# Kernel optimization log

Hardware: AMD Instinct MI355X
Metric: run time of the kernel (lower is better)

Reference implementation:

```python
import jax, jax.numpy as jnp
import numpy as np

ALPHA = 0.2  # LeakyReLU negative slope (module init arg)


def setup_inputs() -> dict:
    key = jax.random.key(0)
    ks = jax.random.split(key, 5)
    b, w, K, E = 8, 256, 256, 512  # batch, window_size, n_features, embed (=2*window)
    x = jax.random.normal(ks[0], (b, w, K), dtype=jnp.float32)
    W = jax.random.normal(ks[1], (E, 2 * w), dtype=jnp.float32) * 0.05
    b_lin = jax.random.normal(ks[2], (E,), dtype=jnp.float32) * 0.05
    a = jax.random.normal(ks[3], (E,), dtype=jnp.float32) * 0.05
    bias = jax.random.normal(ks[4], (K, K), dtype=jnp.float32) * 0.05
    return {"x": x, "W": W, "b_lin": b_lin, "a": a, "bias": bias}


def reference(x, W, b_lin, a, bias):
    # x: (b, window, K) -> v: (b, K, window)
    v = jnp.transpose(x, (0, 2, 1))
    w = v.shape[2]
    # lin(concat(v_i, v_j)) == v_i @ Wl^T + v_j @ Wr^T + b_lin  (split weight)
    Wl, Wr = W[:, :w], W[:, w:]
    left = jnp.einsum('bkw,ew->bke', v, Wl)    # (b, K, E)
    right = jnp.einsum('bkw,ew->bke', v, Wr)   # (b, K, E)
    pre = left[:, :, None, :] + right[:, None, :, :] + b_lin  # (b, K, K, E)
    act = jax.nn.leaky_relu(pre, negative_slope=ALPHA)
    e = jnp.einsum('bije,e->bij', act, a) + bias               # (b, K, K)
    attn = jax.nn.softmax(e, axis=2)  # dropout p=0 in eval -> identity
    h = jax.nn.sigmoid(jnp.einsum('bij,bjw->biw', attn, v))    # (b, K, window)
    return jnp.transpose(h, (0, 2, 1))                          # (b, window, K)
```

## Files before the change

### kernel.cpp

```cpp
#include <hip/hip_runtime.h>
#include <math.h>

typedef float f32x4 __attribute__((ext_vector_type(4)));
typedef __bf16 bf16x8 __attribute__((ext_vector_type(8)));
typedef unsigned short u16x8 __attribute__((ext_vector_type(8)));

__device__ __forceinline__ unsigned short f2bf(float f) {
    union { float f; unsigned int u; } v; v.f = f;
    unsigned int u = v.u;
    return (unsigned short)((u + 0x7fffu + ((u >> 16) & 1u)) >> 16);
}
__device__ __forceinline__ float bf_lo(unsigned int d) {
    union { unsigned int u; float f; } v; v.u = d << 16; return v.f;
}
__device__ __forceinline__ float bf_hi(unsigned int d) {
    union { unsigned int u; float f; } v; v.u = d & 0xffff0000u; return v.f;
}
__device__ __forceinline__ float sigmoidf_(float v) {
    return 1.f / (1.f + __expf(-v));
}

__global__ __launch_bounds__(256) void mfma_gemm_kernel(
    const float* __restrict__ x,
    const float* __restrict__ W,
    const float* __restrict__ b_lin,
    float* __restrict__ Lp,
    unsigned short* __restrict__ R2)
{
    const int b = blockIdx.y;
    const int t = blockIdx.x;
    const bool left = (t < 32);
    int m0, n0;
    if (left) { m0 = (t >> 3) * 64; n0 = (t & 7) * 64; }
    else      { const int tt = t - 32; m0 = (tt >> 2) * 64; n0 = (tt & 3) * 64; }

    __shared__ unsigned short As[64][72];
    __shared__ unsigned short Bs[64][72];

    unsigned short (*Ts)[72] = left ? As : Bs;
    unsigned short (*Ds)[72] = left ? Bs : As;
    const int cbase = left ? m0 : n0;
    const int rbase = left ? n0 : m0;
    const int coff  = left ? 0 : 256;

    const int tid  = threadIdx.x;
    const int wv   = tid >> 6;
    const int lane = tid & 63;
    const int wy = wv >> 1, wx = wv & 1;
    const int lr = lane & 15;
    const int lk = lane >> 4;

    const float* xb = x + b * 65536;

    f32x4 acc[2][2];
    #pragma unroll
    for (int i = 0; i < 2; i++)
        #pragma unroll
        for (int jj = 0; jj < 2; jj++) acc[i][jj] = (f32x4){0.f, 0.f, 0.f, 0.f};

    const int wl = tid >> 4;
    const int kg = tid & 15;
    const int dr = tid >> 2;
    const int dc = (tid & 3) * 16;

    for (int k0 = 0; k0 < 256; k0 += 64) {
        #pragma unroll
        for (int p = 0; p < 4; p++) {
            const int w = wl + 16 * p;
            const float4 v = *(const float4*)(xb + (k0 + w) * 256 + cbase + kg * 4);
            Ts[kg * 4 + 0][w] = f2bf(v.x);
            Ts[kg * 4 + 1][w] = f2bf(v.y);
            Ts[kg * 4 + 2][w] = f2bf(v.z);
            Ts[kg * 4 + 3][w] = f2bf(v.w);
        }
        {
            const float* src = W + (rbase + dr) * 512 + coff + k0 + dc;
            const float4 v0 = *(const float4*)(src);
            const float4 v1 = *(const float4*)(src + 4);
            const float4 v2 = *(const float4*)(src + 8);
            const float4 v3 = *(const float4*)(src + 12);
            u16x8 o0, o1;
            o0[0] = f2bf(v0.x); o0[1] = f2bf(v0.y); o0[2] = f2bf(v0.z); o0[3] = f2bf(v0.w);
            o0[4] = f2bf(v1.x); o0[5] = f2bf(v1.y); o0[6] = f2bf(v1.z); o0[7] = f2bf(v1.w);
            o1[0] = f2bf(v2.x); o1[1] = f2bf(v2.y); o1[2] = f2bf(v2.z); o1[3] = f2bf(v2.w);
            o1[4] = f2bf(v3.x); o1[5] = f2bf(v3.y); o1[6] = f2bf(v3.z); o1[7] = f2bf(v3.w);
            *(u16x8*)&Ds[dr][dc]     = o0;
            *(u16x8*)&Ds[dr][dc + 8] = o1;
        }
        __syncthreads();
        #pragma unroll
        for (int kk = 0; kk < 64; kk += 32) {
            const bf16x8 a0 = *(const bf16x8*)&As[wy * 32 + lr][kk + lk * 8];
            const bf16x8 a1 = *(const bf16x8*)&As[wy * 32 + 16 + lr][kk + lk * 8];
            const bf16x8 b0 = *(const bf16x8*)&Bs[wx * 32 + lr][kk + lk * 8];
            const bf16x8 b1 = *(const bf16x8*)&Bs[wx * 32 + 16 + lr][kk + lk * 8];
            acc[0][0] = __builtin_amdgcn_mfma_f32_16x16x32_bf16(a0, b0, acc[0][0], 0, 0, 0);
            acc[0][1] = __builtin_amdgcn_mfma_f32_16x16x32_bf16(a0, b1, acc[0][1], 0, 0, 0);
            acc[1][0] = __builtin_amdgcn_mfma_f32_16x16x32_bf16(a1, b0, acc[1][0], 0, 0, 0);
            acc[1][1] = __builtin_amdgcn_mfma_f32_16x16x32_bf16(a1, b1, acc[1][1], 0, 0, 0);
        }
        __syncthreads();
    }

    if (left) {
        #pragma unroll
        for (int mi = 0; mi < 2; mi++) {
            #pragma unroll
            for (int ni = 0; ni < 2; ni++) {
                const int row = m0 + wy * 32 + mi * 16 + lk * 4;
                const int col = n0 + wx * 32 + ni * 16 + lr;
                const float bl = b_lin[col];
                #pragma unroll
                for (int r = 0; r < 4; r++)
                    Lp[b * 131072 + (row + r) * 512 + col] = acc[mi][ni][r] + bl;
            }
        }
    } else {
        unsigned short* R2b = R2 + b * 131072;
        #pragma unroll
        for (int mi = 0; mi < 2; mi++) {
            #pragma unroll
            for (int ni = 0; ni < 2; ni++) {
                const int row = m0 + wy * 32 + mi * 16 + lk * 4;
                const int col = n0 + wx * 32 + ni * 16 + lr;
                ushort4 o;
                o.x = f2bf(acc[mi][ni][0]);
                o.y = f2bf(acc[mi][ni][1]);
                o.z = f2bf(acc[mi][ni][2]);
                o.w = f2bf(acc[mi][ni][3]);
                *(ushort4*)(R2b + (row >> 3) * 2048 + col * 8 + (row & 7)) = o;
            }
        }
    }
}

__global__ __launch_bounds__(1024, 4) void attn_kernel(
    const float* __restrict__ x,
    const float* __restrict__ Lp,
    const unsigned int* __restrict__ R2u,
    const float* __restrict__ a,
    const float* __restrict__ bias,
    float* __restrict__ out)
{
    const int b   = blockIdx.x & 7;
    const int i0  = (blockIdx.x >> 3) * 4;
    const int tid = threadIdx.x;
    const int j   = tid & 255;
    const int q   = __builtin_amdgcn_readfirstlane(tid >> 8);

    __shared__ float acc2P[4096];
    __shared__ float rgp[1024];
    __shared__ float atf[1024];
    __shared__ float u15s[4];
    __shared__ unsigned short atbf[16 * 264];

    if (tid < 256) {
        const int i = tid >> 6, lane = tid & 63;
        const float* Lr = Lp + b * 131072 + (i0 + i) * 512 + lane * 8;
        const float* ar = a + lane * 8;
        const float4 la = *(const float4*)Lr;
        const float4 lb = *(const float4*)(Lr + 4);
        const float4 ca = *(const float4*)ar;
        const float4 cb = *(const float4*)(ar + 4);
        float p = la.x * ca.x + la.y * ca.y + la.z * ca.z + la.w * ca.w
                + lb.x * cb.x + lb.y * cb.y + lb.z * cb.z + lb.w * cb.w;
        #pragma unroll
        for (int off = 32; off; off >>= 1) p += __shfl_xor(p, off);
        if (lane == 0) u15s[i] = 0.6f * p;
    }

    const float* Lq = Lp + b * 131072 + i0 * 512 + q * 128;
    const float* aq = a + q * 128;
    const uint4* Rq = (const uint4*)(R2u + b * 65536) + (q * 16) * 256 + j;

    float acc0 = 0.f, acc1 = 0.f, acc2 = 0.f, acc3 = 0.f, rsum = 0.f;

    uint4 cur = Rq[0];
    #pragma unroll 2
    for (int tk = 0; tk < 16; tk++) {
        uint4 nxt;
        if (tk < 15) nxt = Rq[(tk + 1) * 256];
        float r[8];
        r[0] = bf_lo(cur.x); r[1] = bf_hi(cur.x);
        r[2] = bf_lo(cur.y); r[3] = bf_hi(cur.y);
        r[4] = bf_lo(cur.z); r[5] = bf_hi(cur.z);
        r[6] = bf_lo(cur.w); r[7] = bf_hi(cur.w);
        #pragma unroll
        for (int s = 0; s < 8; s++) {
            const int el = tk * 8 + s;
            const float ae = aq[el];
            rsum = fmaf(ae, r[s], rsum);
            const float p0 = Lq[el]        + r[s];
            const float p1 = Lq[512 + el]  + r[s];
            const float p2 = Lq[1024 + el] + r[s];
            const float p3 = Lq[1536 + el] + r[s];
            acc0 = fmaf(ae, fabsf(p0), acc0);
            acc1 = fmaf(ae, fabsf(p1), acc1);
            acc2 = fmaf(ae, fabsf(p2), acc2);
            acc3 = fmaf(ae, fabsf(p3), acc3);
        }
        cur = nxt;
    }
    {
        float* dst = acc2P + q * 1024 + j;
        dst[0]   = acc0;
        dst[256] = acc1;
        dst[512] = acc2;
        dst[768] = acc3;
        rgp[q * 256 + j] = rsum;
    }
    if (tid >= 512 && tid < 768) {
        for (int z = tid - 512; z < 12 * 264; z += 256) atbf[4 * 264 + z] = 0;
    }
    __syncthreads();

    if (tid < 256) {
        const float uR = rgp[j] + rgp[256 + j] + rgp[512 + j] + rgp[768 + j];
        #pragma unroll
        for (int i = 0; i < 4; i++) {
            const float ab = acc2P[i * 256 + j] + acc2P[1024 + i * 256 + j]
                           + acc2P[2048 + i * 256 + j] + acc2P[3072 + i * 256 + j];
            atf[i * 256 + j] = u15s[i] + 0.6f * uR + 0.4f * ab
                             + bias[(i0 + i) * 256 + j];
        }
    }
    __syncthreads();

    if (tid < 256) {
        const int i = tid >> 6, lane = tid & 63;
        float v[4];
        float m = -1e30f;
        #pragma unroll
        for (int u = 0; u < 4; u++) {
            v[u] = atf[i * 256 + lane + 64 * u];
            m = fmaxf(m, v[u]);
        }
        #pragma unroll
        for (int off = 32; off; off >>= 1) m = fmaxf(m, __shfl_xor(m, off));
        float s = 0.f;
        #pragma unroll
        for (int u = 0; u < 4; u++) { v[u] = __expf(v[u] - m); s += v[u]; }
        #pragma unroll
        for (int off = 32; off; off >>= 1) s += __shfl_xor(s, off);
        const float inv = 1.f / s;
        #pragma unroll
        for (int u = 0; u < 4; u++)
            atbf[i * 264 + lane + 64 * u] = f2bf(v[u] * inv);
    }
    __syncthreads();

    {
        const int nt = tid >> 6;
        const int lane = tid & 63;
        const int lr = lane & 15;
        const int lk = lane >> 4;
        f32x4 hacc = (f32x4){0.f, 0.f, 0.f, 0.f};
        const float* xw = x + b * 65536 + (nt * 16 + lr) * 256;
        #pragma unroll
        for (int kt = 0; kt < 8; kt++) {
            const bf16x8 av = *(const bf16x8*)&atbf[lr * 264 + kt * 32 + lk * 8];
            const float4 f0 = *(const float4*)(xw + kt * 32 + lk * 8);
            const float4 f1 = *(const float4*)(xw + kt * 32 + lk * 8 + 4);
            u16x8 bu;
            bu[0] = f2bf(f0.x); bu[1] = f2bf(f0.y); bu[2] = f2bf(f0.z); bu[3] = f2bf(f0.w);
            bu[4] = f2bf(f1.x); bu[5] = f2bf(f1.y); bu[6] = f2bf(f1.z); bu[7] = f2bf(f1.w);
            const bf16x8 bv = *(const bf16x8*)&bu;
            hacc = __builtin_amdgcn_mfma_f32_16x16x32_bf16(av, bv, hacc, 0, 0, 0);
        }
        if (lk == 0) {
            float4 o;
            o.x = sigmoidf_(hacc[0]);
            o.y = sigmoidf_(hacc[1]);
            o.z = sigmoidf_(hacc[2]);
            o.w = sigmoidf_(hacc[3]);
            *(float4*)(out + b * 65536 + (nt * 16 + lr) * 256 + i0) = o;
        }
    }
}

extern "C" void kernel_launch(void* const* d_in, const int* in_sizes, int n_in,
                              void* d_out, int out_size, void* d_ws, size_t ws_size,
                              hipStream_t stream) {
    const float* x     = (const float*)d_in[0];
    const float* W     = (const float*)d_in[1];
    const float* b_lin = (const float*)d_in[2];
    const float* a     = (const float*)d_in[3];
    const float* bias  = (const float*)d_in[4];
    float* out = (float*)d_out;

    char* ws = (char*)d_ws;
    float*          Lp = (float*)ws;
    unsigned short* R2 = (unsigned short*)(ws + (4 << 20));

    mfma_gemm_kernel<<<dim3(64, 8), 256, 0, stream>>>(x, W, b_lin, Lp, R2);
    attn_kernel<<<512, 1024, 0, stream>>>(x, Lp, (const unsigned int*)R2, a, bias, out);
}
```

Baseline: 123.3 us.

## Stage L and a in LDS, halve attn block size with 2-way E split

The attention kernel now runs 512-thread blocks instead of 1024. The E dimension is split two ways instead of four, and each thread walks 256 embedding elements. The four left-projection rows and the vector a are staged into LDS in a transposed [e][i] layout, so one float4 LDS read supplies all four i values instead of four separate global loads. The partial-sum reduction is folded into the softmax step, which drops the atf buffer and a barrier. The output MFMA phase makes each wave handle two 16-column tiles. In exchange, each thread carries a longer serial loop, and the explicit zeroing of the unused atbf rows is gone.

```diff
diff --git a/kernel.cpp b/kernel.cpp
--- a/kernel.cpp
+++ b/kernel.cpp
@@ -134,7 +134,7 @@
     }
 }
 
-__global__ __launch_bounds__(1024, 4) void attn_kernel(
+__global__ __launch_bounds__(512, 8) void attn_kernel(
     const float* __restrict__ x,
     const float* __restrict__ Lp,
     const unsigned int* __restrict__ R2u,
@@ -146,13 +146,25 @@
     const int i0  = (blockIdx.x >> 3) * 4;
     const int tid = threadIdx.x;
     const int j   = tid & 255;
-    const int q   = __builtin_amdgcn_readfirstlane(tid >> 8);
-
-    __shared__ float acc2P[4096];
-    __shared__ float rgp[1024];
-    __shared__ float atf[1024];
+    const int eh  = tid >> 8;
+
+    __shared__ float Lt[512][4];
+    __shared__ float aS[512];
+    __shared__ float acc2P[2][4][256];
+    __shared__ float rgp[2][256];
     __shared__ float u15s[4];
     __shared__ unsigned short atbf[16 * 264];
+
+    {
+        const int i  = tid >> 7;
+        const int e0 = (tid & 127) * 4;
+        const float4 v = *(const float4*)(Lp + b * 131072 + (i0 + i) * 512 + e0);
+        Lt[e0 + 0][i] = v.x;
+        Lt[e0 + 1][i] = v.y;
+        Lt[e0 + 2][i] = v.z;
+        Lt[e0 + 3][i] = v.w;
+        aS[tid] = a[tid];
+    }
 
     if (tid < 256) {
         const int i = tid >> 6, lane = tid & 63;
@@ -168,71 +180,59 @@
         for (int off = 32; off; off >>= 1) p += __shfl_xor(p, off);
         if (lane == 0) u15s[i] = 0.6f * p;
     }
-
-    const float* Lq = Lp + b * 131072 + i0 * 512 + q * 128;
-    const float* aq = a + q * 128;
-    const uint4* Rq = (const uint4*)(R2u + b * 65536) + (q * 16) * 256 + j;
+    __syncthreads();
+
+    const float* aq = aS + eh * 256;
+    const float (*Ltq)[4] = (const float (*)[4])(Lt + eh * 256);
+    const uint4* Rq = (const uint4*)(R2u + b * 65536) + (eh * 32) * 256 + j;
 
     float acc0 = 0.f, acc1 = 0.f, acc2 = 0.f, acc3 = 0.f, rsum = 0.f;
 
     uint4 cur = Rq[0];
-    #pragma unroll 2
-    for (int tk = 0; tk < 16; tk++) {
+    for (int tk = 0; tk < 32; tk++) {
         uint4 nxt;
-        if (tk < 15) nxt = Rq[(tk + 1) * 256];
+        if (tk < 31) nxt = Rq[(tk + 1) * 256];
         float r[8];
         r[0] = bf_lo(cur.x); r[1] = bf_hi(cur.x);
         r[2] = bf_lo(cur.y); r[3] = bf_hi(cur.y);
         r[4] = bf_lo(cur.z); r[5] = bf_hi(cur.z);
         r[6] = bf_lo(cur.w); r[7] = bf_hi(cur.w);
         #pragma unroll
-        for (int s = 0; s < 8; s++) {
-            const int el = tk * 8 + s;
-            const float ae = aq[el];
-            rsum = fmaf(ae, r[s], rsum);
-            const float p0 = Lq[el]        + r[s];
-            const float p1 = Lq[512 + el]  + r[s];
-            const float p2 = Lq[1024 + el] + r[s];
-            const float p3 = Lq[1536 + el] + r[s];
-            acc0 = fmaf(ae, fabsf(p0), acc0);
-            acc1 = fmaf(ae, fabsf(p1), acc1);
-            acc2 = fmaf(ae, fabsf(p2), acc2);
-            acc3 = fmaf(ae, fabsf(p3), acc3);
+        for (int q2 = 0; q2 < 2; q2++) {
+            const float4 av4 = *(const float4*)&aq[tk * 8 + q2 * 4];
+            #pragma unroll
+            for (int s = 0; s < 4; s++) {
+                const int e = tk * 8 + q2 * 4 + s;
+                const float4 lv = *(const float4*)Ltq[e];
+                const float ae = ((const float*)&av4)[s];
+                const float rv = r[q2 * 4 + s];
+                rsum = fmaf(ae, rv, rsum);
+                acc0 = fmaf(ae, fabsf(lv.x + rv), acc0);
+                acc1 = fmaf(ae, fabsf(lv.y + rv), acc1);
+                acc2 = fmaf(ae, fabsf(lv.z + rv), acc2);
+                acc3 = fmaf(ae, fabsf(lv.w + rv), acc3);
+            }
         }
         cur = nxt;
     }
-    {
-        float* dst = acc2P + q * 1024 + j;
-        dst[0]   = acc0;
-        dst[256] = acc1;
-        dst[512] = acc2;
-        dst[768] = acc3;
-        rgp[q * 256 + j] = rsum;
-    }
-    if (tid >= 512 && tid < 768) {
-        for (int z = tid - 512; z < 12 * 264; z += 256) atbf[4 * 264 + z] = 0;
-    }
-    __syncthreads();
-
-    if (tid < 256) {
-        const float uR = rgp[j] + rgp[256 + j] + rgp[512 + j] + rgp[768 + j];
-        #pragma unroll
-        for (int i = 0; i < 4; i++) {
-            const float ab = acc2P[i * 256 + j] + acc2P[1024 + i * 256 + j]
-                           + acc2P[2048 + i * 256 + j] + acc2P[3072 + i * 256 + j];
-            atf[i * 256 + j] = u15s[i] + 0.6f * uR + 0.4f * ab
-                             + bias[(i0 + i) * 256 + j];
-        }
-    }
+    acc2P[eh][0][j] = acc0;
+    acc2P[eh][1][j] = acc1;
+    acc2P[eh][2][j] = acc2;
+    acc2P[eh][3][j] = acc3;
+    rgp[eh][j] = rsum;
     __syncthreads();
 
     if (tid < 256) {
         const int i = tid >> 6, lane = tid & 63;
+        const float u15 = u15s[i];
         float v[4];
         float m = -1e30f;
         #pragma unroll
         for (int u = 0; u < 4; u++) {
-            v[u] = atf[i * 256 + lane + 64 * u];
+            const int jj = lane + 64 * u;
+            const float uR = rgp[0][jj] + rgp[1][jj];
+            const float ab = acc2P[0][i][jj] + acc2P[1][i][jj];
+            v[u] = u15 + 0.6f * uR + 0.4f * ab + bias[(i0 + i) * 256 + jj];
             m = fmaxf(m, v[u]);
         }
         #pragma unroll
@@ -250,30 +250,34 @@
     __syncthreads();
 
     {
-        const int nt = tid >> 6;
+        const int wvv  = tid >> 6;
         const int lane = tid & 63;
         const int lr = lane & 15;
         const int lk = lane >> 4;
-        f32x4 hacc = (f32x4){0.f, 0.f, 0.f, 0.f};
-        const float* xw = x + b * 65536 + (nt * 16 + lr) * 256;
-        #pragma unroll
-        for (int kt = 0; kt < 8; kt++) {
-            const bf16x8 av = *(const bf16x8*)&atbf[lr * 264 + kt * 32 + lk * 8];
-            const float4 f0 = *(const float4*)(xw + kt * 32 + lk * 8);
-            const float4 f1 = *(const float4*)(xw + kt * 32 + lk * 8 + 4);
-            u16x8 bu;
-            bu[0] = f2bf(f0.x); bu[1] = f2bf(f0.y); bu[2] = f2bf(f0.z); bu[3] = f2bf(f0.w);
-            bu[4] = f2bf(f1.x); bu[5] = f2bf(f1.y); bu[6] = f2bf(f1.z); bu[7] = f2bf(f1.w);
-            const bf16x8 bv = *(const bf16x8*)&bu;
-            hacc = __builtin_amdgcn_mfma_f32_16x16x32_bf16(av, bv, hacc, 0, 0, 0);
-        }
-        if (lk == 0) {
-            float4 o;
-            o.x = sigmoidf_(hacc[0]);
-            o.y = sigmoidf_(hacc[1]);
-            o.z = sigmoidf_(hacc[2]);
-            o.w = sigmoidf_(hacc[3]);
-            *(float4*)(out + b * 65536 + (nt * 16 + lr) * 256 + i0) = o;
+        #pragma unroll
+        for (int half = 0; half < 2; half++) {
+            const int nt = wvv + half * 8;
+            f32x4 hacc = (f32x4){0.f, 0.f, 0.f, 0.f};
+            const float* xw = x + b * 65536 + (nt * 16 + lr) * 256;
+            #pragma unroll
+            for (int kt = 0; kt < 8; kt++) {
+                const bf16x8 av = *(const bf16x8*)&atbf[lr * 264 + kt * 32 + lk * 8];
+                const float4 f0 = *(const float4*)(xw + kt * 32 + lk * 8);
+                const float4 f1 = *(const float4*)(xw + kt * 32 + lk * 8 + 4);
+                u16x8 bu;
+                bu[0] = f2bf(f0.x); bu[1] = f2bf(f0.y); bu[2] = f2bf(f0.z); bu[3] = f2bf(f0.w);
+                bu[4] = f2bf(f1.x); bu[5] = f2bf(f1.y); bu[6] = f2bf(f1.z); bu[7] = f2bf(f1.w);
+                const bf16x8 bv = *(const bf16x8*)&bu;
+                hacc = __builtin_amdgcn_mfma_f32_16x16x32_bf16(av, bv, hacc, 0, 0, 0);
+            }
+            if (lk == 0) {
+                float4 o;
+                o.x = sigmoidf_(hacc[0]);
+                o.y = sigmoidf_(hacc[1]);
+                o.z = sigmoidf_(hacc[2]);
+                o.w = sigmoidf_(hacc[3]);
+                *(float4*)(out + b * 65536 + (nt * 16 + lr) * 256 + i0) = o;
+            }
         }
     }
 }
@@ -293,5 +297,5 @@
     unsigned short* R2 = (unsigned short*)(ws + (4 << 20));
 
     mfma_gemm_kernel<<<dim3(64, 8), 256, 0, stream>>>(x, W, b_lin, Lp, R2);
-    attn_kernel<<<512, 1024, 0, stream>>>(x, Lp, (const unsigned int*)R2, a, bias, out);
-}
+    attn_kernel<<<512, 512, 0, stream>>>(x, Lp, (const unsigned int*)R2, a, bias, out);
+}
```

After: 107.8 us. 1.14x faster.
